# Kernel optimization log

Measured on AMD Instinct MI355X. Metric: run time of the kernel, lower is better.

Reference implementation:

```python
import jax, jax.numpy as jnp
import numpy as np

TAU, LBDA, THETA = 0.25, 0.15, 0.3
N_WARPS, N_ITERS = 1, 30
EPS = 1e-12  # GRAD_IS_ZERO

GAUSS = jnp.array([
    [0.000874, 0.006976, 0.01386, 0.006976, 0.000874],
    [0.006976, 0.0557, 0.110656, 0.0557, 0.006976],
    [0.01386, 0.110656, 0.219833, 0.110656, 0.01386],
    [0.006976, 0.0557, 0.110656, 0.0557, 0.006976],
    [0.000874, 0.006976, 0.01386, 0.006976, 0.000874]], dtype=jnp.float32)


def to_gray(x):  # [B,3,H,W] -> [B,1,H,W], BGR-style weights from repo
    w = jnp.array([0.114, 0.587, 0.299], x.dtype)
    return jnp.einsum('bchw,c->bhw', x, w)[:, None]


def normalize_pair(x1, x2):
    mn = jnp.minimum(x1.min(), x2.min())
    mx = jnp.maximum(x1.max(), x2.max())
    den = mx - mn
    return 255.0 * (x1 - mn) / den, 255.0 * (x2 - mn) / den


def gaussian_smooth(x):
    k = GAUSS[None, None].astype(x.dtype)
    return jax.lax.conv_general_dilated(x, k, (1, 1), 'SAME')


def centered_grad(x):  # central differences, one-sided at borders (scaled 0.5)
    dx = jnp.concatenate([0.5 * (x[..., 1:2] - x[..., 0:1]),
                          0.5 * (x[..., 2:] - x[..., :-2]),
                          0.5 * (x[..., -1:] - x[..., -2:-1])], axis=-1)
    dy = jnp.concatenate([0.5 * (x[..., 1:2, :] - x[..., 0:1, :]),
                          0.5 * (x[..., 2:, :] - x[..., :-2, :]),
                          0.5 * (x[..., -1:, :] - x[..., -2:-1, :])], axis=-2)
    return dx, dy


def fwd_grad(x):  # forward differences, zero at last col/row
    dx = jnp.concatenate([x[..., 1:] - x[..., :-1], jnp.zeros_like(x[..., :1])], axis=-1)
    dy = jnp.concatenate([x[..., 1:, :] - x[..., :-1, :], jnp.zeros_like(x[..., :1, :])], axis=-2)
    return dx, dy


def divergence(px, py):  # adjoint of fwd_grad (backward differences with boundary handling)
    xp = jnp.concatenate([jnp.zeros_like(px[..., :1]), px[..., :-1]], axis=-1)
    yp = jnp.concatenate([jnp.zeros_like(py[..., :1, :]), py[..., :-1, :]], axis=-2)
    dx = jnp.concatenate([xp[..., 1:] - xp[..., :-1], -xp[..., -1:]], axis=-1)
    dy = jnp.concatenate([yp[..., 1:, :] - yp[..., :-1, :], -yp[..., -1:, :]], axis=-2)
    return dx + dy


def warp(x, u, v):  # grid_sample bilinear, align_corners=True, zeros padding
    B, C, H, W = x.shape
    base_x = jnp.linspace(-1.0, 1.0, W)[None, None, :]
    base_y = jnp.linspace(-1.0, 1.0, H)[None, :, None]
    gx = base_x + 2.0 * u[:, 0] / W   # [B,H,W]
    gy = base_y + 2.0 * v[:, 0] / H
    ix = (gx + 1.0) * 0.5 * (W - 1)
    iy = (gy + 1.0) * 0.5 * (H - 1)
    ix0 = jnp.floor(ix); iy0 = jnp.floor(iy)
    wx = ix - ix0; wy = iy - iy0

    def gather(yy, xx):
        valid = (xx >= 0) & (xx <= W - 1) & (yy >= 0) & (yy <= H - 1)
        xi = jnp.clip(xx, 0, W - 1).astype(jnp.int32)
        yi = jnp.clip(yy, 0, H - 1).astype(jnp.int32)
        flat = (yi * W + xi).reshape(B, 1, H * W)
        g = jnp.take_along_axis(x.reshape(B, C, H * W), flat, axis=2).reshape(B, C, H, W)
        return g * valid[:, None].astype(x.dtype)

    return (gather(iy0, ix0) * ((1 - wx) * (1 - wy))[:, None]
            + gather(iy0, ix0 + 1) * (wx * (1 - wy))[:, None]
            + gather(iy0 + 1, ix0) * ((1 - wx) * wy)[:, None]
            + gather(iy0 + 1, ix0 + 1) * (wx * wy)[:, None])


def tvnet_scale(x1, x2, u1, u2):
    l_t = LBDA * THETA
    taut = TAU / THETA
    d2x, d2y = centered_grad(x2)
    p11 = jnp.zeros_like(x1); p12 = jnp.zeros_like(x1)
    p21 = jnp.zeros_like(x1); p22 = jnp.zeros_like(x1)
    rho = jnp.zeros_like(x1)
    for _ in range(N_WARPS):
        x2w = warp(x2, u1, u2)
        dxw = warp(d2x, u1, u2)
        dyw = warp(d2y, u1, u2)
        grad = dxw ** 2 + dyw ** 2 + EPS
        rho_c = x2w - dxw * u1 - dyw * u2 - x1

        def body(carry, _):
            u1, u2, p11, p12, p21, p22, _ = carry
            rho = rho_c + dxw * u1 + dyw * u2 + EPS
            th = l_t * grad
            m3 = (rho >= -th) & (rho <= th) & (grad > EPS)
            coef = (jnp.where(rho < -th, l_t, 0.0)
                    + jnp.where(rho > th, -l_t, 0.0)
                    + jnp.where(m3, -rho / grad, 0.0))
            v1 = coef * dxw + u1
            v2 = coef * dyw + u2
            u1n = v1 + THETA * divergence(p11, p12)
            u2n = v2 + THETA * divergence(p21, p22)
            u1x, u1y = fwd_grad(u1n)
            u2x, u2y = fwd_grad(u2n)
            ng1 = 1.0 + taut * jnp.sqrt(u1x ** 2 + u1y ** 2 + EPS)
            ng2 = 1.0 + taut * jnp.sqrt(u2x ** 2 + u2y ** 2 + EPS)
            p11n = (p11 + taut * u1x) / ng1
            p12n = (p12 + taut * u1y) / ng1
            p21n = (p21 + taut * u2x) / ng2
            p22n = (p22 + taut * u2y) / ng2
            return (u1n, u2n, p11n, p12n, p21n, p22n, rho), None

        (u1, u2, p11, p12, p21, p22, rho), _ = jax.lax.scan(
            body, (u1, u2, p11, p12, p21, p22, rho), None, length=N_ITERS)
    return u1, u2, rho


def setup_inputs() -> dict:
    key = jax.random.key(0)
    k1, k2 = jax.random.split(key)
    x1 = jax.random.uniform(k1, (8, 3, 256, 256), dtype=jnp.float32)
    x2 = jax.random.uniform(k2, (8, 3, 256, 256), dtype=jnp.float32)
    return {"x1": x1, "x2": x2}


def reference(x1, x2):
    g1 = to_gray(x1)
    g2 = to_gray(x2)
    n1, n2 = normalize_pair(g1, g2)
    s1 = gaussian_smooth(n1)
    s2 = gaussian_smooth(n2)
    u1 = jnp.zeros_like(s1)
    u2 = jnp.zeros_like(s1)
    u1, u2, rho = tvnet_scale(s1, s2, u1, u2)
    return jnp.concatenate([u1, u2, rho], axis=1)  # [B,3,H,W]
```

## Files before the change

kernel.cpp:

```cpp
#include <hip/hip_runtime.h>
#include <hip/hip_fp16.h>
#include <math.h>

typedef float v2f __attribute__((ext_vector_type(2)));
static __device__ __forceinline__ v2f v2(float a, float b){ v2f r; r.x=a; r.y=b; return r; }
#define PKFMA(a,b,c) __builtin_elementwise_fma((a),(b),(c))

#define HH 256
#define WW 256
#define BB 8
#define NPIX (BB*HH*WW)
#define HWPLANE (HH*WW)
#define EPSF 1e-12f

#define TS 32
#define HL 6
#define SS (TS + 2*HL)
#define SS2 (SS*SS)
#define NTH 1024
#define NPR (SS2/2)
#define OWNBIT (1<<13)

#define GSS (TS + 6)
#define GSS2 (GSS*GSS)
#define S2S (TS + 2)
#define S2S2 (S2S*S2S)

constexpr float L_T   = (float)(0.15*0.3);
constexpr float TAUT  = (float)(0.25/0.3);
constexpr float THETA = 0.3f;

static __device__ __constant__ float GK[25] = {
  0.000874f, 0.006976f, 0.01386f,  0.006976f, 0.000874f,
  0.006976f, 0.0557f,   0.110656f, 0.0557f,   0.006976f,
  0.01386f,  0.110656f, 0.219833f, 0.110656f, 0.01386f,
  0.006976f, 0.0557f,   0.110656f, 0.0557f,   0.006976f,
  0.000874f, 0.006976f, 0.01386f,  0.006976f, 0.000874f };


__global__ void k_gray_minmax(const float* __restrict__ x1, const float* __restrict__ x2,
                              float* __restrict__ g1, float* __restrict__ g2,
                              unsigned int* __restrict__ mnmx) {
    __shared__ float smn[4], smx[4];
    float mn = 1e30f, mx = -1e30f;
    int stride = gridDim.x * blockDim.x;
    const int NV = 2*NPIX/4;
    for (int v = blockIdx.x*blockDim.x + threadIdx.x; v < NV; v += stride) {
        int img = v >> 17;
        int rem = v & (NPIX/4 - 1);
        const float* x = img ? x2 : x1;
        float* g = img ? g2 : g1;
        int b = rem >> 14;
        int pix = (rem & (HWPLANE/4 - 1)) << 2;
        const float* base = x + (size_t)b*3*HWPLANE + pix;
        float4 c0 = *(const float4*)(base);
        float4 c1 = *(const float4*)(base + HWPLANE);
        float4 c2 = *(const float4*)(base + 2*HWPLANE);
        float4 gr;
        gr.x = 0.114f*c0.x + 0.587f*c1.x + 0.299f*c2.x;
        gr.y = 0.114f*c0.y + 0.587f*c1.y + 0.299f*c2.y;
        gr.z = 0.114f*c0.z + 0.587f*c1.z + 0.299f*c2.z;
        gr.w = 0.114f*c0.w + 0.587f*c1.w + 0.299f*c2.w;
        *(float4*)(g + ((size_t)rem << 2)) = gr;
        mn = fminf(mn, fminf(fminf(gr.x, gr.y), fminf(gr.z, gr.w)));
        mx = fmaxf(mx, fmaxf(fmaxf(gr.x, gr.y), fmaxf(gr.z, gr.w)));
    }
    #pragma unroll
    for (int off = 32; off; off >>= 1) {
        mn = fminf(mn, __shfl_down(mn, off, 64));
        mx = fmaxf(mx, __shfl_down(mx, off, 64));
    }
    int wid = threadIdx.x >> 6;
    if ((threadIdx.x & 63) == 0) { smn[wid] = mn; smx[wid] = mx; }
    __syncthreads();
    if (threadIdx.x == 0) {
        mn = fminf(fminf(smn[0], smn[1]), fminf(smn[2], smn[3]));
        mx = fmaxf(fmaxf(smx[0], smx[1]), fmaxf(smx[2], smx[3]));
        atomicMin(&mnmx[0], __float_as_uint(mn));
        atomicMax((int*)&mnmx[1], (int)__float_as_uint(mx));
    }
}

__global__ void __launch_bounds__(256)
k_smooth_grad(const float* __restrict__ g1, const float* __restrict__ g2,
              const unsigned int* __restrict__ mnmx, float4* __restrict__ dxr) {
    __shared__ float gn1[GSS2], gn2[GSS2], s2L[S2S2];
    const int blk   = blockIdx.x;
    const int plane = blk >> 6;
    const int t     = blk & 63;
    const int oy0   = (t >> 3) << 5;
    const int ox0   = (t & 7) << 5;
    const int pbse  = plane * HWPLANE;
    const int tid   = threadIdx.x;

    const float mn  = __uint_as_float(mnmx[0]);
    const float inv = 255.0f / (__uint_as_float(mnmx[1]) - mn);

    for (int s = tid; s < GSS2; s += 256) {
        int sy = s / GSS, sx = s - sy*GSS;
        int gy = oy0 - 3 + sy, gx = ox0 - 3 + sx;
        bool im = (gx >= 0) & (gx < WW) & (gy >= 0) & (gy < HH);
        int gi = pbse + gy*WW + gx;
        gn1[s] = im ? (g1[gi] - mn)*inv : 0.f;
        gn2[s] = im ? (g2[gi] - mn)*inv : 0.f;
    }
    __syncthreads();

    for (int c = tid; c < S2S2; c += 256) {
        int sy = c / S2S, sx = c - sy*S2S;
        const float* gb = gn2 + sy*GSS + sx;
        float acc = 0.f;
        #pragma unroll
        for (int i = 0; i < 5; ++i)
            #pragma unroll
            for (int j = 0; j < 5; ++j)
                acc += gb[i*GSS + j] * GK[i*5 + j];
        s2L[c] = acc;
    }
    float s1r[4];
    #pragma unroll
    for (int i = 0; i < 4; ++i) {
        int c = tid + i*256;
        int oy = c >> 5, ox = c & 31;
        const float* gb = gn1 + (oy+1)*GSS + (ox+1);
        float acc = 0.f;
        #pragma unroll
        for (int ii = 0; ii < 5; ++ii)
            #pragma unroll
            for (int jj = 0; jj < 5; ++jj)
                acc += gb[ii*GSS + jj] * GK[ii*5 + jj];
        s1r[i] = acc;
    }
    __syncthreads();

    #pragma unroll
    for (int i = 0; i < 4; ++i) {
        int c = tid + i*256;
        int oy = c >> 5, ox = c & 31;
        int gy = oy0 + oy, gx = ox0 + ox;
        int sc = (oy+1)*S2S + (ox+1);
        float s2c = s2L[sc];
        float xp = (gx < WW-1) ? s2L[sc+1]    : s2c;
        float xm = (gx > 0)    ? s2L[sc-1]    : s2c;
        float yp = (gy < HH-1) ? s2L[sc+S2S]  : s2c;
        float ym = (gy > 0)    ? s2L[sc-S2S]  : s2c;
        float dx = 0.5f*(xp - xm), dy = 0.5f*(yp - ym);
        float grad = fmaf(dx, dx, fmaf(dy, dy, EPSF));
        float rgr  = __builtin_amdgcn_rcpf(grad);
        dxr[pbse + gy*WW + gx] = make_float4(dx, dy, s2c - s1r[i], rgr);
    }
}

__global__ void __launch_bounds__(NTH)
k_iter6(float* __restrict__ F, float* __restrict__ out, int itbase) {
    const float4* DXR = (const float4*)F;
    const int j  = itbase / HL;
    const int rd = j & 1;
    const uint4* Xr = (const uint4*)(F + (size_t)NPIX*(rd ? 12 : 6));
    uint4*       Xw = (uint4*)(F + (size_t)NPIX*(rd ? 6 : 12));

    __shared__ v2f u12[SS2];
    __shared__ v2f pa [SS2];
    __shared__ v2f pb [SS2];

    const int blk   = blockIdx.x;
    const int plane = blk >> 6;
    const int t     = blk & 63;
    const int gy0   = ((t >> 3) << 5) - HL;
    const int gx0   = ((t & 7) << 5) - HL;
    const int pbse  = plane * HWPLANE;
    const int tid   = threadIdx.x;
    const int sxmax = WW-1 - gx0;
    const int symax = HH-1 - gy0;

    int ccP = 0;
    v2f dv[2]; float rcv[2], rgr[2];
    v2f ru[2], rpa[2], rpb[2];

    if (tid < NPR) {
        int ku0=0,ku1=0, kp0=0,kp1=0, ow0=0;
        #pragma unroll
        for (int i = 0; i < 2; ++i) {
            dv[i]=v2(0.f,0.f); rcv[i]=EPSF; rgr[i]=0.f;
            ru[i]=v2(0.f,0.f); rpa[i]=v2(0.f,0.f); rpb[i]=v2(0.f,0.f);
            int s = 2*tid + i;
            int sy = s / SS, sx = s - sy*SS;
            int gy = gy0 + sy, gx = gx0 + sx;
            bool im = (gx >= 0) & (gx < WW) & (gy >= 0) & (gy < HH);
            if (im) {
                int m  = min(min(sy-1, sx-1), min(SS-1-sy, SS-1-sx));
                int mp = min(m, min(SS-2-sy, SS-2-sx));
                int ku = max(m,  -1) + 1;
                int kp = max(mp, -1) + 1;
                int ow = (int)((sy >= HL) & (sy < HL+TS) & (sx >= HL) & (sx < HL+TS));
                if (i == 0) { ku0=ku; kp0=kp; ow0=ow; }
                else        { ku1=ku; kp1=kp; ow0|=ow; }
                int gi = pbse + gy*WW + gx;
                float4 dvv = DXR[gi];
                dv[i] = v2(dvv.x, dvv.y); rcv[i] = dvv.z + EPSF; rgr[i] = dvv.w;
                if (itbase) {
                    uint4 xv = Xr[gi];
                    float2 uf = __half22float2(*(__half2*)&xv.x);
                    float2 af = __half22float2(*(__half2*)&xv.y);
                    float2 bf = __half22float2(*(__half2*)&xv.z);
                    ru[i]=v2(uf.x,uf.y); rpa[i]=v2(af.x,af.y); rpb[i]=v2(bf.x,bf.y);
                }
            }
        }
        int s0 = 2*tid, sy0 = s0 / SS, sx0 = s0 - sy0*SS;
        ccP = (max(kp0,kp1) << 24) | (max(ku0,ku1) << 16)
            | (ow0 ? OWNBIT : 0) | (sy0 << 6) | sx0;
        *(float4*)&u12[s0] = make_float4(ru[0].x,ru[0].y,ru[1].x,ru[1].y);
        *(float4*)&pa [s0] = make_float4(rpa[0].x,rpa[0].y,rpa[1].x,rpa[1].y);
        *(float4*)&pb [s0] = make_float4(rpb[0].x,rpb[0].y,rpb[1].x,rpb[1].y);
    }
    __syncthreads();

    #pragma unroll 1
    for (int k = 0; k < HL; ++k) {
        const bool lastk = (k == HL-1);
        const bool it29  = (itbase + k == 29);

        if (k < ((ccP >> 16) & 0xFF)) {
            int s0 = 2*tid;
            v2f pal0 = pa[s0-1];
            float4 pb2 = *(const float4*)&pb[s0-SS];
            float rho0 = fmaf(dv[0].x, ru[0].x, fmaf(dv[0].y, ru[0].y, rcv[0]));
            float rho1 = fmaf(dv[1].x, ru[1].x, fmaf(dv[1].y, ru[1].y, rcv[1]));
            float co0 = fminf(fmaxf(-rho0 * rgr[0], -L_T), L_T);
            float co1 = fminf(fmaxf(-rho1 * rgr[1], -L_T), L_T);
            v2f d0 = (rpa[0] - pal0)   + (rpb[0] - v2(pb2.x,pb2.y));
            v2f d1 = (rpa[1] - rpa[0]) + (rpb[1] - v2(pb2.z,pb2.w));
            v2f un0 = PKFMA(v2(THETA,THETA), d0, PKFMA(v2(co0,co0), dv[0], ru[0]));
            v2f un1 = PKFMA(v2(THETA,THETA), d1, PKFMA(v2(co1,co1), dv[1], ru[1]));
            if (it29) {
                if (ccP & OWNBIT) {
                    int sy = (ccP >> 6) & 63, sx = ccP & 63;
                    float2* o = (float2*)(out + (size_t)plane*3*HWPLANE + (gy0+sy)*WW + (gx0+sx));
                    o[0]         = make_float2(un0.x, un1.x);
                    o[HWPLANE/2] = make_float2(un0.y, un1.y);
                    o[HWPLANE]   = make_float2(rho0, rho1);
                }
            } else {
                ru[0] = un0; ru[1] = un1;
                *(float4*)&u12[s0] = make_float4(un0.x,un0.y,un1.x,un1.y);
            }
        }
        if (it29) return;
        __syncthreads();

        if (k < (int)((unsigned)ccP >> 24)) {
            int s0 = 2*tid;
            int sy = (ccP >> 6) & 63, sx = ccP & 63;
            float fdm  = (sy     < symax) ? 1.f : 0.f;
            float fbm0 = (sx     < sxmax) ? 1.f : 0.f;
            float fbm1 = (sx + 1 < sxmax) ? 1.f : 0.f;
            v2f ur1 = u12[s0+2];
            float4 ud2 = *(const float4*)&u12[s0+SS];
            v2f ux0 = (ru[1] - ru[0]) * fbm0;
            v2f uy0 = (v2(ud2.x,ud2.y) - ru[0]) * fdm;
            v2f ux1 = (ur1 - ru[1]) * fbm1;
            v2f uy1 = (v2(ud2.z,ud2.w) - ru[1]) * fdm;
            v2f q0 = PKFMA(ux0, ux0, PKFMA(uy0, uy0, v2(EPSF,EPSF)));
            v2f q1 = PKFMA(ux1, ux1, PKFMA(uy1, uy1, v2(EPSF,EPSF)));
            v2f ng0 = PKFMA(v2(TAUT,TAUT), v2(__builtin_amdgcn_sqrtf(q0.x),__builtin_amdgcn_sqrtf(q0.y)), v2(1.f,1.f));
            v2f ng1 = PKFMA(v2(TAUT,TAUT), v2(__builtin_amdgcn_sqrtf(q1.x),__builtin_amdgcn_sqrtf(q1.y)), v2(1.f,1.f));
            v2f r0 = v2(__builtin_amdgcn_rcpf(ng0.x), __builtin_amdgcn_rcpf(ng0.y));
            v2f r1 = v2(__builtin_amdgcn_rcpf(ng1.x), __builtin_amdgcn_rcpf(ng1.y));
            rpa[0] = PKFMA(v2(TAUT,TAUT), ux0, rpa[0]) * r0;
            rpb[0] = PKFMA(v2(TAUT,TAUT), uy0, rpb[0]) * r0;
            rpa[1] = PKFMA(v2(TAUT,TAUT), ux1, rpa[1]) * r1;
            rpb[1] = PKFMA(v2(TAUT,TAUT), uy1, rpb[1]) * r1;
            if (!lastk) {
                *(float4*)&pa[s0] = make_float4(rpa[0].x,rpa[0].y,rpa[1].x,rpa[1].y);
                *(float4*)&pb[s0] = make_float4(rpb[0].x,rpb[0].y,rpb[1].x,rpb[1].y);
            } else if (ccP & OWNBIT) {
                int gi = pbse + (gy0+sy)*WW + (gx0+sx);
                __half2 h0u = __floats2half2_rn(ru[0].x, ru[0].y);
                __half2 h0a = __floats2half2_rn(rpa[0].x, rpa[0].y);
                __half2 h0b = __floats2half2_rn(rpb[0].x, rpb[0].y);
                __half2 h1u = __floats2half2_rn(ru[1].x, ru[1].y);
                __half2 h1a = __floats2half2_rn(rpa[1].x, rpa[1].y);
                __half2 h1b = __floats2half2_rn(rpb[1].x, rpb[1].y);
                uint4 x0, x1;
                x0.x = *(unsigned int*)&h0u; x0.y = *(unsigned int*)&h0a;
                x0.z = *(unsigned int*)&h0b; x0.w = 0u;
                x1.x = *(unsigned int*)&h1u; x1.y = *(unsigned int*)&h1a;
                x1.z = *(unsigned int*)&h1b; x1.w = 0u;
                Xw[gi]   = x0;
                Xw[gi+1] = x1;
            }
        }
        if (!lastk) __syncthreads();
    }
}

extern "C" void kernel_launch(void* const* d_in, const int* in_sizes, int n_in,
                              void* d_out, int out_size, void* d_ws, size_t ws_size,
                              hipStream_t stream) {
    const float* x1 = (const float*)d_in[0];
    const float* x2 = (const float*)d_in[1];
    float* out = (float*)d_out;

    char* ws = (char*)d_ws;
    unsigned int* mnmx = (unsigned int*)ws;
    float* F = (float*)(ws + 256);
    float4* dxr = (float4*)F;
    float*  g1  = F + 4*(size_t)NPIX;
    float*  g2  = F + 5*(size_t)NPIX;

    k_gray_minmax<<<dim3(512), dim3(256), 0, stream>>>(x1, x2, g1, g2, mnmx);
    k_smooth_grad<<<dim3(512), dim3(256), 0, stream>>>(g1, g2, mnmx, dxr);

    for (int itbase = 0; itbase < 30; itbase += HL)
        k_iter6<<<dim3(512), dim3(NTH), 0, stream>>>(F, out, itbase);
}
```

Baseline: 144.3 us.

## Merge u and p update phases with redundant neighbor recompute and ping-pong LDS

Each thread now recomputes the updated u of its right and down neighbours from the old double-buffered shared state, so the p update can run right after the u update without a barrier in between. This removes one __syncthreads per inner iteration. In exchange it adds redundant arithmetic, extra LDS reads, extra global loads of neighbour coefficients, and doubles shared memory, which may lower occupancy.

```diff
diff --git a/kernel.cpp b/kernel.cpp
--- a/kernel.cpp
+++ b/kernel.cpp
@@ -159,9 +159,9 @@
     const uint4* Xr = (const uint4*)(F + (size_t)NPIX*(rd ? 12 : 6));
     uint4*       Xw = (uint4*)(F + (size_t)NPIX*(rd ? 6 : 12));
 
-    __shared__ v2f u12[SS2];
-    __shared__ v2f pa [SS2];
-    __shared__ v2f pb [SS2];
+    __shared__ v2f u12[2*SS2];
+    __shared__ v2f pa [2*SS2];
+    __shared__ v2f pb [2*SS2];
 
     const int blk   = blockIdx.x;
     const int plane = blk >> 6;
@@ -176,7 +176,16 @@
     int ccP = 0;
     v2f dv[2]; float rcv[2], rgr[2];
     v2f ru[2], rpa[2], rpb[2];
-
+    v2f dvR;   float rcvR, rgrR;
+    v2f dvD[2]; float rcvD[2], rgrD[2];
+
+    for (int s = tid; s < 2*SS2; s += NTH) {
+        u12[s] = v2(0.f,0.f); pa[s] = v2(0.f,0.f); pb[s] = v2(0.f,0.f);
+    }
+    __syncthreads();
+
+    dvR = v2(0.f,0.f); rcvR = EPSF; rgrR = 0.f;
+    dvD[0] = dvD[1] = v2(0.f,0.f); rcvD[0] = rcvD[1] = EPSF; rgrD[0] = rgrD[1] = 0.f;
     if (tid < NPR) {
         int ku0=0,ku1=0, kp0=0,kp1=0, ow0=0;
         #pragma unroll
@@ -210,6 +219,29 @@
         int s0 = 2*tid, sy0 = s0 / SS, sx0 = s0 - sy0*SS;
         ccP = (max(kp0,kp1) << 24) | (max(ku0,ku1) << 16)
             | (ow0 ? OWNBIT : 0) | (sy0 << 6) | sx0;
+        {
+            int sR = s0 + 2;
+            if (sR < SS2) {
+                int sy = sR / SS, sx = sR - sy*SS;
+                int gy = gy0 + sy, gx = gx0 + sx;
+                if ((gx >= 0) & (gx < WW) & (gy >= 0) & (gy < HH)) {
+                    float4 dvv = DXR[pbse + gy*WW + gx];
+                    dvR = v2(dvv.x, dvv.y); rcvR = dvv.z + EPSF; rgrR = dvv.w;
+                }
+            }
+            #pragma unroll
+            for (int i = 0; i < 2; ++i) {
+                int sD = s0 + SS + i;
+                if (sD < SS2) {
+                    int sy = sD / SS, sx = sD - sy*SS;
+                    int gy = gy0 + sy, gx = gx0 + sx;
+                    if ((gx >= 0) & (gx < WW) & (gy >= 0) & (gy < HH)) {
+                        float4 dvv = DXR[pbse + gy*WW + gx];
+                        dvD[i] = v2(dvv.x, dvv.y); rcvD[i] = dvv.z + EPSF; rgrD[i] = dvv.w;
+                    }
+                }
+            }
+        }
         *(float4*)&u12[s0] = make_float4(ru[0].x,ru[0].y,ru[1].x,ru[1].y);
         *(float4*)&pa [s0] = make_float4(rpa[0].x,rpa[0].y,rpa[1].x,rpa[1].y);
         *(float4*)&pb [s0] = make_float4(rpb[0].x,rpb[0].y,rpb[1].x,rpb[1].y);
@@ -220,11 +252,13 @@
     for (int k = 0; k < HL; ++k) {
         const bool lastk = (k == HL-1);
         const bool it29  = (itbase + k == 29);
+        const int RB = (k & 1) ? SS2 : 0;
+        const int WB = SS2 - RB;
+        const int s0 = 2*tid;
 
         if (k < ((ccP >> 16) & 0xFF)) {
-            int s0 = 2*tid;
-            v2f pal0 = pa[s0-1];
-            float4 pb2 = *(const float4*)&pb[s0-SS];
+            v2f pal0 = pa[RB + s0 - 1];
+            float4 pb2 = *(const float4*)&pb[RB + s0 - SS];
             float rho0 = fmaf(dv[0].x, ru[0].x, fmaf(dv[0].y, ru[0].y, rcv[0]));
             float rho1 = fmaf(dv[1].x, ru[1].x, fmaf(dv[1].y, ru[1].y, rcv[1]));
             float co0 = fminf(fmaxf(-rho0 * rgr[0], -L_T), L_T);
@@ -243,54 +277,72 @@
                 }
             } else {
                 ru[0] = un0; ru[1] = un1;
-                *(float4*)&u12[s0] = make_float4(un0.x,un0.y,un1.x,un1.y);
+                *(float4*)&u12[WB + s0] = make_float4(un0.x,un0.y,un1.x,un1.y);
+
+                if (k < (int)((unsigned)ccP >> 24)) {
+                    v2f paRc = pa[RB + s0 + 2];
+                    v2f pbRc = pb[RB + s0 + 2];
+                    float4 pbru = *(const float4*)&pb[RB + s0 - SS + 2];
+                    v2f uoR  = u12[RB + s0 + 2];
+                    float rhoR = fmaf(dvR.x, uoR.x, fmaf(dvR.y, uoR.y, rcvR));
+                    float coR  = fminf(fmaxf(-rhoR * rgrR, -L_T), L_T);
+                    v2f dR = (paRc - rpa[1]) + (pbRc - v2(pbru.x,pbru.y));
+                    v2f huR = PKFMA(v2(THETA,THETA), dR, PKFMA(v2(coR,coR), dvR, uoR));
+                    v2f palD = pa[RB + s0 + SS - 1];
+                    float4 paD = *(const float4*)&pa[RB + s0 + SS];
+                    float4 pbD = *(const float4*)&pb[RB + s0 + SS];
+                    float4 uoD = *(const float4*)&u12[RB + s0 + SS];
+                    v2f uoD0 = v2(uoD.x,uoD.y), uoD1 = v2(uoD.z,uoD.w);
+                    float rhoD0 = fmaf(dvD[0].x, uoD0.x, fmaf(dvD[0].y, uoD0.y, rcvD[0]));
+                    float rhoD1 = fmaf(dvD[1].x, uoD1.x, fmaf(dvD[1].y, uoD1.y, rcvD[1]));
+                    float coD0 = fminf(fmaxf(-rhoD0 * rgrD[0], -L_T), L_T);
+                    float coD1 = fminf(fmaxf(-rhoD1 * rgrD[1], -L_T), L_T);
+                    v2f dD0 = (v2(paD.x,paD.y) - palD)          + (v2(pbD.x,pbD.y) - rpb[0]);
+                    v2f dD1 = (v2(paD.z,paD.w) - v2(paD.x,paD.y)) + (v2(pbD.z,pbD.w) - rpb[1]);
+                    v2f huD0 = PKFMA(v2(THETA,THETA), dD0, PKFMA(v2(coD0,coD0), dvD[0], uoD0));
+                    v2f huD1 = PKFMA(v2(THETA,THETA), dD1, PKFMA(v2(coD1,coD1), dvD[1], uoD1));
+
+                    int sy = (ccP >> 6) & 63, sx = ccP & 63;
+                    float fdm  = (sy     < symax) ? 1.f : 0.f;
+                    float fbm0 = (sx     < sxmax) ? 1.f : 0.f;
+                    float fbm1 = (sx + 1 < sxmax) ? 1.f : 0.f;
+                    v2f ux0 = (un1 - un0) * fbm0;
+                    v2f uy0 = (huD0 - un0) * fdm;
+                    v2f ux1 = (huR - un1) * fbm1;
+                    v2f uy1 = (huD1 - un1) * fdm;
+                    v2f q0 = PKFMA(ux0, ux0, PKFMA(uy0, uy0, v2(EPSF,EPSF)));
+                    v2f q1 = PKFMA(ux1, ux1, PKFMA(uy1, uy1, v2(EPSF,EPSF)));
+                    v2f ng0 = PKFMA(v2(TAUT,TAUT), v2(__builtin_amdgcn_sqrtf(q0.x),__builtin_amdgcn_sqrtf(q0.y)), v2(1.f,1.f));
+                    v2f ng1 = PKFMA(v2(TAUT,TAUT), v2(__builtin_amdgcn_sqrtf(q1.x),__builtin_amdgcn_sqrtf(q1.y)), v2(1.f,1.f));
+                    v2f r0 = v2(__builtin_amdgcn_rcpf(ng0.x), __builtin_amdgcn_rcpf(ng0.y));
+                    v2f r1 = v2(__builtin_amdgcn_rcpf(ng1.x), __builtin_amdgcn_rcpf(ng1.y));
+                    rpa[0] = PKFMA(v2(TAUT,TAUT), ux0, rpa[0]) * r0;
+                    rpb[0] = PKFMA(v2(TAUT,TAUT), uy0, rpb[0]) * r0;
+                    rpa[1] = PKFMA(v2(TAUT,TAUT), ux1, rpa[1]) * r1;
+                    rpb[1] = PKFMA(v2(TAUT,TAUT), uy1, rpb[1]) * r1;
+                    if (!lastk) {
+                        *(float4*)&pa[WB + s0] = make_float4(rpa[0].x,rpa[0].y,rpa[1].x,rpa[1].y);
+                        *(float4*)&pb[WB + s0] = make_float4(rpb[0].x,rpb[0].y,rpb[1].x,rpb[1].y);
+                    } else if (ccP & OWNBIT) {
+                        int gi = pbse + (gy0+sy)*WW + (gx0+sx);
+                        __half2 h0u = __floats2half2_rn(ru[0].x, ru[0].y);
+                        __half2 h0a = __floats2half2_rn(rpa[0].x, rpa[0].y);
+                        __half2 h0b = __floats2half2_rn(rpb[0].x, rpb[0].y);
+                        __half2 h1u = __floats2half2_rn(ru[1].x, ru[1].y);
+                        __half2 h1a = __floats2half2_rn(rpa[1].x, rpa[1].y);
+                        __half2 h1b = __floats2half2_rn(rpb[1].x, rpb[1].y);
+                        uint4 x0, x1;
+                        x0.x = *(unsigned int*)&h0u; x0.y = *(unsigned int*)&h0a;
+                        x0.z = *(unsigned int*)&h0b; x0.w = 0u;
+                        x1.x = *(unsigned int*)&h1u; x1.y = *(unsigned int*)&h1a;
+                        x1.z = *(unsigned int*)&h1b; x1.w = 0u;
+                        Xw[gi]   = x0;
+                        Xw[gi+1] = x1;
+                    }
+                }
             }
         }
         if (it29) return;
-        __syncthreads();
-
-        if (k < (int)((unsigned)ccP >> 24)) {
-            int s0 = 2*tid;
-            int sy = (ccP >> 6) & 63, sx = ccP & 63;
-            float fdm  = (sy     < symax) ? 1.f : 0.f;
-            float fbm0 = (sx     < sxmax) ? 1.f : 0.f;
-            float fbm1 = (sx + 1 < sxmax) ? 1.f : 0.f;
-            v2f ur1 = u12[s0+2];
-            float4 ud2 = *(const float4*)&u12[s0+SS];
-            v2f ux0 = (ru[1] - ru[0]) * fbm0;
-            v2f uy0 = (v2(ud2.x,ud2.y) - ru[0]) * fdm;
-            v2f ux1 = (ur1 - ru[1]) * fbm1;
-            v2f uy1 = (v2(ud2.z,ud2.w) - ru[1]) * fdm;
-            v2f q0 = PKFMA(ux0, ux0, PKFMA(uy0, uy0, v2(EPSF,EPSF)));
-            v2f q1 = PKFMA(ux1, ux1, PKFMA(uy1, uy1, v2(EPSF,EPSF)));
-            v2f ng0 = PKFMA(v2(TAUT,TAUT), v2(__builtin_amdgcn_sqrtf(q0.x),__builtin_amdgcn_sqrtf(q0.y)), v2(1.f,1.f));
-            v2f ng1 = PKFMA(v2(TAUT,TAUT), v2(__builtin_amdgcn_sqrtf(q1.x),__builtin_amdgcn_sqrtf(q1.y)), v2(1.f,1.f));
-            v2f r0 = v2(__builtin_amdgcn_rcpf(ng0.x), __builtin_amdgcn_rcpf(ng0.y));
-            v2f r1 = v2(__builtin_amdgcn_rcpf(ng1.x), __builtin_amdgcn_rcpf(ng1.y));
-            rpa[0] = PKFMA(v2(TAUT,TAUT), ux0, rpa[0]) * r0;
-            rpb[0] = PKFMA(v2(TAUT,TAUT), uy0, rpb[0]) * r0;
-            rpa[1] = PKFMA(v2(TAUT,TAUT), ux1, rpa[1]) * r1;
-            rpb[1] = PKFMA(v2(TAUT,TAUT), uy1, rpb[1]) * r1;
-            if (!lastk) {
-                *(float4*)&pa[s0] = make_float4(rpa[0].x,rpa[0].y,rpa[1].x,rpa[1].y);
-                *(float4*)&pb[s0] = make_float4(rpb[0].x,rpb[0].y,rpb[1].x,rpb[1].y);
-            } else if (ccP & OWNBIT) {
-                int gi = pbse + (gy0+sy)*WW + (gx0+sx);
-                __half2 h0u = __floats2half2_rn(ru[0].x, ru[0].y);
-                __half2 h0a = __floats2half2_rn(rpa[0].x, rpa[0].y);
-                __half2 h0b = __floats2half2_rn(rpb[0].x, rpb[0].y);
-                __half2 h1u = __floats2half2_rn(ru[1].x, ru[1].y);
-                __half2 h1a = __floats2half2_rn(rpa[1].x, rpa[1].y);
-                __half2 h1b = __floats2half2_rn(rpb[1].x, rpb[1].y);
-                uint4 x0, x1;
-                x0.x = *(unsigned int*)&h0u; x0.y = *(unsigned int*)&h0a;
-                x0.z = *(unsigned int*)&h0b; x0.w = 0u;
-                x1.x = *(unsigned int*)&h1u; x1.y = *(unsigned int*)&h1a;
-                x1.z = *(unsigned int*)&h1b; x1.w = 0u;
-                Xw[gi]   = x0;
-                Xw[gi+1] = x1;
-            }
-        }
         if (!lastk) __syncthreads();
     }
 }
```

After: 180.5 us. 25.1% more time.
